# Performance work log

Measured on AMD Instinct MI355X. Metric: run time of the kernel, lower is better.

The kernel has to match this reference:

```python
import jax, jax.numpy as jnp
import numpy as np
from jax import lax

B = 256; C_IN = 12; H = 84; W = 84
HID = 1024; NC = 16; NE = 512; EPC = 64
FLAT = 64 * 7 * 7  # encoder output size for 84x84 input


def setup_inputs() -> dict:
    key = jax.random.key(0)
    ks = jax.random.split(key, 16)
    s = 0.02
    inp = {
        "obs": jax.random.normal(ks[0], (B, C_IN, H, W), dtype=jnp.float32),
        "k1": jax.random.normal(ks[1], (32, C_IN, 8, 8), dtype=jnp.float32) * s,
        "cb1": jnp.zeros((32,), jnp.float32),
        "k2": jax.random.normal(ks[2], (64, 32, 4, 4), dtype=jnp.float32) * s,
        "cb2": jnp.zeros((64,), jnp.float32),
        "k3": jax.random.normal(ks[3], (64, 64, 3, 3), dtype=jnp.float32) * s,
        "cb3": jnp.zeros((64,), jnp.float32),
        "Wproj": jax.random.normal(ks[4], (FLAT, HID), dtype=jnp.float32) * s,
        "bproj": jnp.zeros((HID,), jnp.float32),
        "Wcat": jax.random.normal(ks[5], (HID, NC), dtype=jnp.float32) * s,
        "bcat": jnp.zeros((NC,), jnp.float32),
        "W1": jax.random.normal(ks[6], (NC, HID, HID // 2), dtype=jnp.float32) * s,
        "b1": jnp.zeros((NC, HID // 2), jnp.float32),
        "W2": jax.random.normal(ks[7], (NC, HID // 2, EPC), dtype=jnp.float32) * s,
        "b2": jnp.zeros((NC, EPC), jnp.float32),
        "mapping": jax.random.randint(ks[8], (NC, EPC), 0, NE, dtype=jnp.int64)
        if jax.config.jax_enable_x64 else jax.random.randint(ks[8], (NC, EPC), 0, NE, dtype=jnp.int32),
    }
    return inp


def _conv(x, k, b, stride):
    y = lax.conv_general_dilated(x, k, (stride, stride), "VALID",
                                 dimension_numbers=("NCHW", "OIHW", "NCHW"))
    return y + b[None, :, None, None]


def reference(obs, k1, cb1, k2, cb2, k3, cb3, Wproj, bproj, Wcat, bcat,
              W1, b1, W2, b2, mapping):
    # --- CNN encoder ---
    x = jax.nn.relu(_conv(obs, k1, cb1, 4))   # [B,32,20,20]
    x = jax.nn.relu(_conv(x, k2, cb2, 2))     # [B,64,9,9]
    x = jax.nn.relu(_conv(x, k3, cb3, 1))     # [B,64,7,7]
    feats = x.reshape(x.shape[0], -1)          # [B,3136]

    hidden = jax.nn.relu(feats @ Wproj + bproj)          # [B,HID]
    category_logits = hidden @ Wcat + bcat               # [B,NC]
    category_probs = jax.nn.softmax(category_logits, axis=-1)

    # --- batched per-category expert heads (fused) ---
    h1 = jax.nn.relu(jnp.einsum("bh,chm->bcm", hidden, W1) + b1)   # [B,NC,HID/2]
    local = jax.nn.sigmoid(jnp.einsum("bcm,cme->bce", h1, W2) + b2)  # [B,NC,EPC]
    weighted = category_probs[:, :, None] * local                    # [B,NC,EPC]

    # scatter-add into global expert buffer; mapping [NC,EPC] broadcasts to [B,NC,EPC]
    expert_probs = jnp.zeros((hidden.shape[0], NE), hidden.dtype)
    expert_probs = expert_probs.at[:, mapping].add(weighted)

    return category_logits, expert_probs, hidden
```

## Files before the change

### kernel.cpp

```cpp
#include <hip/hip_runtime.h>
#include <hip/hip_bf16.h>


#define B_    256
#define CIN   12
#define HH    84
#define WW    84
#define HID   1024
#define NC    16
#define NE    512
#define EPC   64
#define FLAT  3136

typedef short short8 __attribute__((ext_vector_type(8)));
typedef short short4_t __attribute__((ext_vector_type(4)));
typedef float f32x4 __attribute__((ext_vector_type(4)));

__device__ __forceinline__ short f2bf(float x) {
    unsigned int u = __float_as_uint(x);
    u = (u + 0x7FFFu + ((u >> 16) & 1u)) >> 16;
    return (short)u;
}

__global__ __launch_bounds__(256) void prep_weights_kernel(
        const float* __restrict__ k1, const float* __restrict__ k2,
        const float* __restrict__ k3, short* __restrict__ k1bf,
        short* __restrict__ k2t, short* __restrict__ k3t) {
    int i = blockIdx.x * 256 + threadIdx.x;
    if (i < 24576) {
        k1bf[i] = f2bf(k1[i]);
    } else if (i < 24576 + 32768) {
        int j = i - 24576;
        int oc = j >> 9, rem = j & 511, tap = rem >> 5, ic = rem & 31;
        k2t[j] = f2bf(k2[oc * 512 + ic * 16 + tap]);
    } else if (i < 24576 + 32768 + 36864) {
        int j = i - 57344;
        int oc = j / 576, rem = j % 576, tap = rem >> 6, ic = rem & 63;
        k3t[j] = f2bf(k3[oc * 576 + ic * 9 + tap]);
    }
}

__global__ __launch_bounds__(256) void transpose_cast_kernel(
        const float* __restrict__ src, short* __restrict__ dst,
        int R, int C, long sbs, long dbs) {
    __shared__ float tile[32][33];
    const int c0 = blockIdx.x * 32, r0 = blockIdx.y * 32, z = blockIdx.z;
    const int tx = threadIdx.x & 31, ty = threadIdx.x >> 5;
    const float* s = src + (size_t)z * sbs;
    short* d = dst + (size_t)z * dbs;
    #pragma unroll
    for (int it = 0; it < 4; ++it)
        tile[ty + it * 8][tx] = s[(size_t)(r0 + ty + it * 8) * C + c0 + tx];
    __syncthreads();
    #pragma unroll
    for (int it = 0; it < 4; ++it) {
        int j = ty + it * 8;
        d[(size_t)(c0 + j) * R + r0 + tx] = f2bf(tile[tx][j]);
    }
}

__global__ __launch_bounds__(448) void conv1_mfma_kernel(
        const float* __restrict__ obs, const short* __restrict__ k1bf,
        const float* __restrict__ cb1, short* __restrict__ x1bf) {
    __shared__ short slab[CIN][24][88];
    const int oyq = blockIdx.x, b = blockIdx.y;
    const int tid = threadIdx.x;

    const float* src = obs + (size_t)b * (CIN * HH * WW) + (20 * oyq) * WW;
    for (int l = tid; l < CIN * 24 * 21; l += 448) {
        int ic = l / 504, rem = l % 504, r = rem / 21, c4 = rem % 21;
        float4 f = *(const float4*)(src + (size_t)ic * (HH * WW) + r * WW + 4 * c4);
        short4_t v;
        v[0] = f2bf(f.x); v[1] = f2bf(f.y); v[2] = f2bf(f.z); v[3] = f2bf(f.w);
        *(short4_t*)&slab[ic][r][4 * c4] = v;
    }
    __syncthreads();

    const int w = tid >> 6, l = tid & 63, lr = l & 15, g = l >> 4;
    const int p = w * 16 + lr;
    const int pw = (p < 100) ? p : 99;
    const int oy_l = pw / 20, ox = pw % 20;
    const short* bb0 = k1bf + lr * 768;
    const short* bb1 = k1bf + (16 + lr) * 768;

    f32x4 acc0 = {0.f, 0.f, 0.f, 0.f}, acc1 = {0.f, 0.f, 0.f, 0.f};
    #pragma unroll 4
    for (int s = 0; s < 24; ++s) {
        const int idx = s * 4 + g;
        const int ic = idx >> 3, ky = idx & 7;
        const short* ap = &slab[ic][4 * oy_l + ky][4 * ox];
        short8 a;
        *(short4_t*)&a       = *(const short4_t*)ap;
        *((short4_t*)&a + 1) = *(const short4_t*)(ap + 4);
        short8 b0 = *(const short8*)(bb0 + s * 32 + g * 8);
        short8 b1 = *(const short8*)(bb1 + s * 32 + g * 8);
        acc0 = __builtin_amdgcn_mfma_f32_16x16x32_bf16(a, b0, acc0, 0, 0, 0);
        acc1 = __builtin_amdgcn_mfma_f32_16x16x32_bf16(a, b1, acc1, 0, 0, 0);
    }
    const float c0v = cb1[lr], c1v = cb1[16 + lr];
    #pragma unroll
    for (int r = 0; r < 4; ++r) {
        const int ro = w * 16 + g * 4 + r;
        if (ro < 100) {
            const int oy_g = 5 * oyq + ro / 20, ox_g = ro % 20;
            short* dst = x1bf + ((size_t)(b * 20 + oy_g) * 20 + ox_g) * 32;
            dst[lr]      = f2bf(fmaxf(acc0[r] + c0v, 0.f));
            dst[16 + lr] = f2bf(fmaxf(acc1[r] + c1v, 0.f));
        }
    }
}

__global__ __launch_bounds__(64) void conv2_mfma_kernel(
        const short* __restrict__ x1bf, const short* __restrict__ k2t,
        const float* __restrict__ cb2, short* __restrict__ x2bf) {
    const int l = threadIdx.x, lr = l & 15, g = l >> 4;
    const int mfb = blockIdx.x * 16;
    const int ro = mfb + lr;
    const int b = ro / 81, pp = ro % 81, oy = pp / 9, ox = pp % 9;
    const short* abase = x1bf + (size_t)b * 12800;

    f32x4 acc[4] = {};
    #pragma unroll 4
    for (int s = 0; s < 16; ++s) {
        const int ky = s >> 2, kx = s & 3;
        short8 a = *(const short8*)(abase +
            ((size_t)((2 * oy + ky) * 20 + 2 * ox + kx)) * 32 + g * 8);
        #pragma unroll
        for (int nf = 0; nf < 4; ++nf) {
            short8 bv = *(const short8*)(k2t + (size_t)(nf * 16 + lr) * 512 + s * 32 + g * 8);
            acc[nf] = __builtin_amdgcn_mfma_f32_16x16x32_bf16(a, bv, acc[nf], 0, 0, 0);
        }
    }
    #pragma unroll
    for (int nf = 0; nf < 4; ++nf) {
        const int col = nf * 16 + lr;
        const float bb = cb2[col];
        #pragma unroll
        for (int r = 0; r < 4; ++r) {
            const int roo = mfb + g * 4 + r;
            x2bf[(size_t)roo * 64 + col] = f2bf(fmaxf(acc[nf][r] + bb, 0.f));
        }
    }
}

__global__ __launch_bounds__(64) void conv3_mfma_kernel(
        const short* __restrict__ x2bf, const short* __restrict__ k3t,
        const float* __restrict__ cb3, short* __restrict__ featsbf) {
    const int l = threadIdx.x, lr = l & 15, g = l >> 4;
    const int mfb = blockIdx.x * 16;
    const int ro = mfb + lr;
    const int b = ro / 49, pp = ro % 49, oy = pp / 7, ox = pp % 7;
    const short* abase = x2bf + (size_t)b * 5184;

    f32x4 acc[4] = {};
    #pragma unroll 4
    for (int s = 0; s < 18; ++s) {
        const int tap = s >> 1, ich = s & 1;
        const int ky = tap / 3, kx = tap % 3;
        short8 a = *(const short8*)(abase +
            ((size_t)((oy + ky) * 9 + ox + kx)) * 64 + ich * 32 + g * 8);
        #pragma unroll
        for (int nf = 0; nf < 4; ++nf) {
            short8 bv = *(const short8*)(k3t + (size_t)(nf * 16 + lr) * 576 + s * 32 + g * 8);
            acc[nf] = __builtin_amdgcn_mfma_f32_16x16x32_bf16(a, bv, acc[nf], 0, 0, 0);
        }
    }
    #pragma unroll
    for (int nf = 0; nf < 4; ++nf) {
        const int col = nf * 16 + lr;
        const float bb = cb3[col];
        #pragma unroll
        for (int r = 0; r < 4; ++r) {
            const int roo = mfb + g * 4 + r;
            const int b_o = roo / 49, p_o = roo % 49;
            featsbf[(size_t)b_o * FLAT + col * 49 + p_o] =
                f2bf(fmaxf(acc[nf][r] + bb, 0.f));
        }
    }
}

__global__ __launch_bounds__(64) void proj_mfma_kernel(
        const short* __restrict__ Abf, const short* __restrict__ Wt,
        const float* __restrict__ bproj, float* __restrict__ hidden,
        short* __restrict__ hbf) {
    const int l = threadIdx.x, lr = l & 15, g = l >> 4;
    const int n0 = blockIdx.x * 16, m0 = blockIdx.y * 32;
    const short* a0 = Abf + (size_t)(m0 + lr) * FLAT;
    const short* a1 = Abf + (size_t)(m0 + 16 + lr) * FLAT;
    const short* br = Wt + (size_t)(n0 + lr) * FLAT;

    f32x4 acc0 = {}, acc1 = {};
    #pragma unroll 4
    for (int s = 0; s < 98; ++s) {
        const int k = s * 32 + g * 8;
        short8 bv = *(const short8*)(br + k);
        short8 av0 = *(const short8*)(a0 + k);
        short8 av1 = *(const short8*)(a1 + k);
        acc0 = __builtin_amdgcn_mfma_f32_16x16x32_bf16(av0, bv, acc0, 0, 0, 0);
        acc1 = __builtin_amdgcn_mfma_f32_16x16x32_bf16(av1, bv, acc1, 0, 0, 0);
    }
    const int col = n0 + lr;
    const float bb = bproj[col];
    #pragma unroll
    for (int r = 0; r < 4; ++r) {
        const int m = m0 + g * 4 + r;
        float v = fmaxf(acc0[r] + bb, 0.f);
        hidden[(size_t)m * HID + col] = v;
        hbf[(size_t)m * HID + col] = f2bf(v);
        const int m2 = m + 16;
        float v2 = fmaxf(acc1[r] + bb, 0.f);
        hidden[(size_t)m2 * HID + col] = v2;
        hbf[(size_t)m2 * HID + col] = f2bf(v2);
    }
}

__global__ __launch_bounds__(256) void cat_softmax_kernel(
        const float* __restrict__ hidden, const float* __restrict__ Wcat,
        const float* __restrict__ bcat, float* __restrict__ logits,
        float* __restrict__ probs) {
    __shared__ float red[256];
    __shared__ float lvals[16];
    const int b = blockIdx.x, tid = threadIdx.x;
    const int cc = tid & 15, kq = tid >> 4;
    const float* hrow = hidden + (size_t)b * HID;
    float p = 0.f;
    for (int t = 0; t < 64; ++t) {
        int k = kq * 64 + t;
        p += hrow[k] * Wcat[k * NC + cc];
    }
    red[tid] = p;
    __syncthreads();
    if (tid < 16) {
        float s = bcat[tid];
        #pragma unroll
        for (int q = 0; q < 16; ++q) s += red[q * 16 + tid];
        logits[b * NC + tid] = s;
        lvals[tid] = s;
    }
    __syncthreads();
    if (tid < 16) {
        float m = lvals[0];
        #pragma unroll
        for (int q = 1; q < 16; ++q) m = fmaxf(m, lvals[q]);
        float sum = 0.f;
        #pragma unroll
        for (int q = 0; q < 16; ++q) sum += expf(lvals[q] - m);
        probs[b * NC + tid] = expf(lvals[tid] - m) / sum;
    }
}

__global__ __launch_bounds__(64) void expert1_mfma_kernel(
        const short* __restrict__ Hbf, const short* __restrict__ W1t,
        const float* __restrict__ b1, short* __restrict__ h1bf) {
    const int l = threadIdx.x, lr = l & 15, g = l >> 4;
    const int n0 = blockIdx.x * 32, m0 = blockIdx.y * 64, c = blockIdx.z;
    const short* ar[4];
    #pragma unroll
    for (int i = 0; i < 4; ++i) ar[i] = Hbf + (size_t)(m0 + i * 16 + lr) * HID;
    const short* br0 = W1t + (size_t)c * (512 * HID) + (size_t)(n0 + lr) * HID;
    const short* br1 = br0 + 16 * HID;

    f32x4 acc[4][2] = {};
    #pragma unroll 2
    for (int s = 0; s < 32; ++s) {
        const int k = s * 32 + g * 8;
        short8 b0 = *(const short8*)(br0 + k);
        short8 b1v = *(const short8*)(br1 + k);
        #pragma unroll
        for (int i = 0; i < 4; ++i) {
            short8 a = *(const short8*)(ar[i] + k);
            acc[i][0] = __builtin_amdgcn_mfma_f32_16x16x32_bf16(a, b0, acc[i][0], 0, 0, 0);
            acc[i][1] = __builtin_amdgcn_mfma_f32_16x16x32_bf16(a, b1v, acc[i][1], 0, 0, 0);
        }
    }
    #pragma unroll
    for (int j = 0; j < 2; ++j) {
        const int col = n0 + j * 16 + lr;
        const float bb = b1[c * 512 + col];
        #pragma unroll
        for (int i = 0; i < 4; ++i)
            #pragma unroll
            for (int r = 0; r < 4; ++r) {
                const int m = m0 + i * 16 + g * 4 + r;
                h1bf[((size_t)c * B_ + m) * 512 + col] =
                    f2bf(fmaxf(acc[i][j][r] + bb, 0.f));
            }
    }
}

__global__ __launch_bounds__(64) void expert2_mfma_kernel(
        const short* __restrict__ h1bf, const short* __restrict__ W2t,
        const float* __restrict__ b2, const float* __restrict__ probs,
        const int* __restrict__ mapping, float* __restrict__ outexp) {
    const int l = threadIdx.x, lr = l & 15, g = l >> 4;
    const int mfb = blockIdx.x * 16, c = blockIdx.y;
    const short* ar = h1bf + ((size_t)c * B_ + mfb + lr) * 512;
    const short* wb = W2t + (size_t)c * (EPC * 512);

    f32x4 acc[4] = {};
    #pragma unroll 4
    for (int s = 0; s < 16; ++s) {
        const int k = s * 32 + g * 8;
        short8 a = *(const short8*)(ar + k);
        #pragma unroll
        for (int nf = 0; nf < 4; ++nf) {
            short8 bv = *(const short8*)(wb + (size_t)(nf * 16 + lr) * 512 + k);
            acc[nf] = __builtin_amdgcn_mfma_f32_16x16x32_bf16(a, bv, acc[nf], 0, 0, 0);
        }
    }
    #pragma unroll
    for (int nf = 0; nf < 4; ++nf) {
        const int e = nf * 16 + lr;
        const float bb = b2[c * EPC + e];
        const int tgt = mapping[c * EPC + e];
        #pragma unroll
        for (int r = 0; r < 4; ++r) {
            const int m = mfb + g * 4 + r;
            const float v = probs[m * NC + c] / (1.f + expf(-(acc[nf][r] + bb)));
            atomicAdd(&outexp[(size_t)m * NE + tgt], v);
        }
    }
}

extern "C" void kernel_launch(void* const* d_in, const int* in_sizes, int n_in,
                              void* d_out, int out_size, void* d_ws, size_t ws_size,
                              hipStream_t stream) {
    const float* obs   = (const float*)d_in[0];
    const float* k1    = (const float*)d_in[1];
    const float* cb1   = (const float*)d_in[2];
    const float* k2    = (const float*)d_in[3];
    const float* cb2   = (const float*)d_in[4];
    const float* k3    = (const float*)d_in[5];
    const float* cb3   = (const float*)d_in[6];
    const float* Wproj = (const float*)d_in[7];
    const float* bproj = (const float*)d_in[8];
    const float* Wcat  = (const float*)d_in[9];
    const float* bcat  = (const float*)d_in[10];
    const float* W1    = (const float*)d_in[11];
    const float* b1    = (const float*)d_in[12];
    const float* W2    = (const float*)d_in[13];
    const float* b2    = (const float*)d_in[14];
    const int*   mapping = (const int*)d_in[15];

    float* out    = (float*)d_out;
    float* logits = out;
    float* outexp = out + B_ * NC;
    float* hidden = out + B_ * NC + B_ * NE;

    char* ws = (char*)d_ws;
    short* x1bf    = (short*)ws;
    short* Wprojt  = (short*)ws;
    short* W1t     = (short*)ws;
    short* W2t     = (short*)ws;
    short* x2bf    = (short*)(ws + 6553600);
    short* featsbf = (short*)(ws + 9207808);
    short* hidbf   = (short*)(ws + 16777216);
    float* probs   = (float*)(ws + 17301504);
    short* k1bf    = (short*)(ws + 17317888);
    short* k2t     = (short*)(ws + 17367040);
    short* k3t     = (short*)(ws + 17432576);
    short* h1bf    = (short*)(ws + 17506304);

    hipMemsetAsync(outexp, 0, (size_t)B_ * NE * sizeof(float), stream);

    prep_weights_kernel<<<dim3(368), 256, 0, stream>>>(k1, k2, k3, k1bf, k2t, k3t);
    conv1_mfma_kernel<<<dim3(4, B_), 448, 0, stream>>>(obs, k1bf, cb1, x1bf);
    conv2_mfma_kernel<<<dim3(1296), 64, 0, stream>>>(x1bf, k2t, cb2, x2bf);
    transpose_cast_kernel<<<dim3(32, 98, 1), 256, 0, stream>>>(
        Wproj, Wprojt, FLAT, HID, 0, 0);
    conv3_mfma_kernel<<<dim3(784), 64, 0, stream>>>(x2bf, k3t, cb3, featsbf);
    proj_mfma_kernel<<<dim3(64, 8), 64, 0, stream>>>(featsbf, Wprojt, bproj, hidden, hidbf);
    cat_softmax_kernel<<<dim3(B_), 256, 0, stream>>>(hidden, Wcat, bcat, logits, probs);
    transpose_cast_kernel<<<dim3(16, 32, 16), 256, 0, stream>>>(
        W1, W1t, HID, 512, (long)HID * 512, (long)HID * 512);
    expert1_mfma_kernel<<<dim3(16, 4, 16), 64, 0, stream>>>(hidbf, W1t, b1, h1bf);
    transpose_cast_kernel<<<dim3(2, 16, 16), 256, 0, stream>>>(
        W2, W2t, 512, EPC, (long)512 * EPC, (long)512 * EPC);
    expert2_mfma_kernel<<<dim3(16, 16), 64, 0, stream>>>(
        h1bf, W2t, b2, probs, mapping, outexp);
}
```

Measured before the change: 373.7 us.

## Split-K the projection GEMM, shrink expert tiles, batch conv1 slab loads

The projection GEMM is split into 8 K-chunks over a 3D grid that atomically accumulate into a zeroed fp32 buffer. A new epilogue kernel then applies bias, ReLU and the bf16 cast. Expert1 and expert2 use smaller per-block tiles so more blocks run in parallel. Conv1's slab load issues seven float4 loads before converting and storing, to raise memory-level parallelism. The cost is an extra memset, an extra kernel launch, atomic traffic, less register reuse per block, and split-K results that are no longer bitwise deterministic.

Result: no change. 375.7 us (+0.5%).

```diff
diff --git a/kernel.cpp b/kernel.cpp
--- a/kernel.cpp
+++ b/kernel.cpp
@@ -67,12 +67,30 @@
     const int tid = threadIdx.x;
 
     const float* src = obs + (size_t)b * (CIN * HH * WW) + (20 * oyq) * WW;
-    for (int l = tid; l < CIN * 24 * 21; l += 448) {
-        int ic = l / 504, rem = l % 504, r = rem / 21, c4 = rem % 21;
-        float4 f = *(const float4*)(src + (size_t)ic * (HH * WW) + r * WW + 4 * c4);
-        short4_t v;
-        v[0] = f2bf(f.x); v[1] = f2bf(f.y); v[2] = f2bf(f.z); v[3] = f2bf(f.w);
-        *(short4_t*)&slab[ic][r][4 * c4] = v;
+    short* sl = &slab[0][0][0];
+    #pragma unroll
+    for (int ph = 0; ph < 2; ++ph) {
+        float4 v[7];
+        int dsti[7];
+        #pragma unroll
+        for (int it = 0; it < 7; ++it) {
+            int l = ph * 3136 + it * 448 + tid;
+            int ok = (l < 6048);
+            int li = ok ? l : 6047;
+            int ic = li / 504, rem = li - ic * 504;
+            int r = rem / 21, c4 = rem - r * 21;
+            v[it] = *(const float4*)(src + (size_t)ic * (HH * WW) + r * WW + 4 * c4);
+            dsti[it] = ok ? (ic * (24 * 88) + r * 88 + 4 * c4) : -1;
+        }
+        #pragma unroll
+        for (int it = 0; it < 7; ++it) {
+            if (dsti[it] >= 0) {
+                short4_t s4v;
+                s4v[0] = f2bf(v[it].x); s4v[1] = f2bf(v[it].y);
+                s4v[2] = f2bf(v[it].z); s4v[3] = f2bf(v[it].w);
+                *(short4_t*)(sl + dsti[it]) = s4v;
+            }
+        }
     }
     __syncthreads();
 
@@ -181,37 +199,45 @@
 
 __global__ __launch_bounds__(64) void proj_mfma_kernel(
         const short* __restrict__ Abf, const short* __restrict__ Wt,
-        const float* __restrict__ bproj, float* __restrict__ hidden,
-        short* __restrict__ hbf) {
+        float* __restrict__ haccum) {
     const int l = threadIdx.x, lr = l & 15, g = l >> 4;
-    const int n0 = blockIdx.x * 16, m0 = blockIdx.y * 32;
-    const short* a0 = Abf + (size_t)(m0 + lr) * FLAT;
-    const short* a1 = Abf + (size_t)(m0 + 16 + lr) * FLAT;
-    const short* br = Wt + (size_t)(n0 + lr) * FLAT;
-
-    f32x4 acc0 = {}, acc1 = {};
-    #pragma unroll 4
-    for (int s = 0; s < 98; ++s) {
+    const int n0 = blockIdx.x * 64, m0 = blockIdx.y * 16;
+    const int kz = blockIdx.z;
+    const int s0 = (kz * 98) >> 3, s1 = ((kz + 1) * 98) >> 3;
+    const short* ar = Abf + (size_t)(m0 + lr) * FLAT;
+    const short* br0 = Wt + (size_t)(n0 + lr) * FLAT;
+
+    f32x4 acc[4] = {};
+    #pragma unroll 2
+    for (int s = s0; s < s1; ++s) {
         const int k = s * 32 + g * 8;
-        short8 bv = *(const short8*)(br + k);
-        short8 av0 = *(const short8*)(a0 + k);
-        short8 av1 = *(const short8*)(a1 + k);
-        acc0 = __builtin_amdgcn_mfma_f32_16x16x32_bf16(av0, bv, acc0, 0, 0, 0);
-        acc1 = __builtin_amdgcn_mfma_f32_16x16x32_bf16(av1, bv, acc1, 0, 0, 0);
-    }
-    const int col = n0 + lr;
-    const float bb = bproj[col];
-    #pragma unroll
-    for (int r = 0; r < 4; ++r) {
-        const int m = m0 + g * 4 + r;
-        float v = fmaxf(acc0[r] + bb, 0.f);
-        hidden[(size_t)m * HID + col] = v;
-        hbf[(size_t)m * HID + col] = f2bf(v);
-        const int m2 = m + 16;
-        float v2 = fmaxf(acc1[r] + bb, 0.f);
-        hidden[(size_t)m2 * HID + col] = v2;
-        hbf[(size_t)m2 * HID + col] = f2bf(v2);
-    }
+        short8 a = *(const short8*)(ar + k);
+        #pragma unroll
+        for (int nf = 0; nf < 4; ++nf) {
+            short8 bv = *(const short8*)(br0 + (size_t)nf * 16 * FLAT + k);
+            acc[nf] = __builtin_amdgcn_mfma_f32_16x16x32_bf16(a, bv, acc[nf], 0, 0, 0);
+        }
+    }
+    #pragma unroll
+    for (int nf = 0; nf < 4; ++nf)
+        #pragma unroll
+        for (int r = 0; r < 4; ++r)
+            atomicAdd(&haccum[(size_t)(m0 + g * 4 + r) * HID + n0 + nf * 16 + lr],
+                      acc[nf][r]);
+}
+
+__global__ __launch_bounds__(256) void proj_epi2_kernel(
+        const float* __restrict__ haccum, const float* __restrict__ bproj,
+        float* __restrict__ hidden, short* __restrict__ hbf) {
+    const int i = blockIdx.x * 256 + threadIdx.x;
+    float4 v = *(const float4*)&haccum[4 * i];
+    float4 bb = *(const float4*)&bproj[(4 * i) & (HID - 1)];
+    float4 r;
+    r.x = fmaxf(v.x + bb.x, 0.f); r.y = fmaxf(v.y + bb.y, 0.f);
+    r.z = fmaxf(v.z + bb.z, 0.f); r.w = fmaxf(v.w + bb.w, 0.f);
+    *(float4*)&hidden[4 * i] = r;
+    short4_t h; h[0] = f2bf(r.x); h[1] = f2bf(r.y); h[2] = f2bf(r.z); h[3] = f2bf(r.w);
+    *(short4_t*)&hbf[4 * i] = h;
 }
 
 __global__ __launch_bounds__(256) void cat_softmax_kernel(
@@ -253,32 +279,31 @@
         const short* __restrict__ Hbf, const short* __restrict__ W1t,
         const float* __restrict__ b1, short* __restrict__ h1bf) {
     const int l = threadIdx.x, lr = l & 15, g = l >> 4;
-    const int n0 = blockIdx.x * 32, m0 = blockIdx.y * 64, c = blockIdx.z;
-    const short* ar[4];
-    #pragma unroll
-    for (int i = 0; i < 4; ++i) ar[i] = Hbf + (size_t)(m0 + i * 16 + lr) * HID;
+    const int n0 = blockIdx.x * 32, m0 = blockIdx.y * 32, c = blockIdx.z;
+    const short* ar0 = Hbf + (size_t)(m0 + lr) * HID;
+    const short* ar1 = ar0 + (size_t)16 * HID;
     const short* br0 = W1t + (size_t)c * (512 * HID) + (size_t)(n0 + lr) * HID;
-    const short* br1 = br0 + 16 * HID;
-
-    f32x4 acc[4][2] = {};
-    #pragma unroll 2
+    const short* br1 = br0 + (size_t)16 * HID;
+
+    f32x4 acc[2][2] = {};
+    #pragma unroll 4
     for (int s = 0; s < 32; ++s) {
         const int k = s * 32 + g * 8;
-        short8 b0 = *(const short8*)(br0 + k);
+        short8 a0 = *(const short8*)(ar0 + k);
+        short8 a1 = *(const short8*)(ar1 + k);
+        short8 b0v = *(const short8*)(br0 + k);
         short8 b1v = *(const short8*)(br1 + k);
-        #pragma unroll
-        for (int i = 0; i < 4; ++i) {
-            short8 a = *(const short8*)(ar[i] + k);
-            acc[i][0] = __builtin_amdgcn_mfma_f32_16x16x32_bf16(a, b0, acc[i][0], 0, 0, 0);
-            acc[i][1] = __builtin_amdgcn_mfma_f32_16x16x32_bf16(a, b1v, acc[i][1], 0, 0, 0);
-        }
+        acc[0][0] = __builtin_amdgcn_mfma_f32_16x16x32_bf16(a0, b0v, acc[0][0], 0, 0, 0);
+        acc[0][1] = __builtin_amdgcn_mfma_f32_16x16x32_bf16(a0, b1v, acc[0][1], 0, 0, 0);
+        acc[1][0] = __builtin_amdgcn_mfma_f32_16x16x32_bf16(a1, b0v, acc[1][0], 0, 0, 0);
+        acc[1][1] = __builtin_amdgcn_mfma_f32_16x16x32_bf16(a1, b1v, acc[1][1], 0, 0, 0);
     }
     #pragma unroll
     for (int j = 0; j < 2; ++j) {
         const int col = n0 + j * 16 + lr;
         const float bb = b1[c * 512 + col];
         #pragma unroll
-        for (int i = 0; i < 4; ++i)
+        for (int i = 0; i < 2; ++i)
             #pragma unroll
             for (int r = 0; r < 4; ++r) {
                 const int m = m0 + i * 16 + g * 4 + r;
@@ -293,32 +318,26 @@
         const float* __restrict__ b2, const float* __restrict__ probs,
         const int* __restrict__ mapping, float* __restrict__ outexp) {
     const int l = threadIdx.x, lr = l & 15, g = l >> 4;
-    const int mfb = blockIdx.x * 16, c = blockIdx.y;
-    const short* ar = h1bf + ((size_t)c * B_ + mfb + lr) * 512;
-    const short* wb = W2t + (size_t)c * (EPC * 512);
-
-    f32x4 acc[4] = {};
+    const int m0 = blockIdx.x * 16, n0 = blockIdx.y * 16, c = blockIdx.z;
+    const short* ar = h1bf + ((size_t)c * B_ + m0 + lr) * 512;
+    const short* br = W2t + (size_t)c * (EPC * 512) + (size_t)(n0 + lr) * 512;
+
+    f32x4 acc = {};
     #pragma unroll 4
     for (int s = 0; s < 16; ++s) {
         const int k = s * 32 + g * 8;
         short8 a = *(const short8*)(ar + k);
-        #pragma unroll
-        for (int nf = 0; nf < 4; ++nf) {
-            short8 bv = *(const short8*)(wb + (size_t)(nf * 16 + lr) * 512 + k);
-            acc[nf] = __builtin_amdgcn_mfma_f32_16x16x32_bf16(a, bv, acc[nf], 0, 0, 0);
-        }
-    }
-    #pragma unroll
-    for (int nf = 0; nf < 4; ++nf) {
-        const int e = nf * 16 + lr;
-        const float bb = b2[c * EPC + e];
-        const int tgt = mapping[c * EPC + e];
-        #pragma unroll
-        for (int r = 0; r < 4; ++r) {
-            const int m = mfb + g * 4 + r;
-            const float v = probs[m * NC + c] / (1.f + expf(-(acc[nf][r] + bb)));
-            atomicAdd(&outexp[(size_t)m * NE + tgt], v);
-        }
+        short8 bv = *(const short8*)(br + k);
+        acc = __builtin_amdgcn_mfma_f32_16x16x32_bf16(a, bv, acc, 0, 0, 0);
+    }
+    const int e = n0 + lr;
+    const float bb = b2[c * EPC + e];
+    const int tgt = mapping[c * EPC + e];
+    #pragma unroll
+    for (int r = 0; r < 4; ++r) {
+        const int m = m0 + g * 4 + r;
+        const float v = probs[m * NC + c] / (1.f + expf(-(acc[r] + bb)));
+        atomicAdd(&outexp[(size_t)m * NE + tgt], v);
     }
 }
 
@@ -353,6 +372,7 @@
     short* W1t     = (short*)ws;
     short* W2t     = (short*)ws;
     short* x2bf    = (short*)(ws + 6553600);
+    float* haccum  = (float*)(ws + 6553600);
     short* featsbf = (short*)(ws + 9207808);
     short* hidbf   = (short*)(ws + 16777216);
     float* probs   = (float*)(ws + 17301504);
@@ -369,13 +389,15 @@
     transpose_cast_kernel<<<dim3(32, 98, 1), 256, 0, stream>>>(
         Wproj, Wprojt, FLAT, HID, 0, 0);
     conv3_mfma_kernel<<<dim3(784), 64, 0, stream>>>(x2bf, k3t, cb3, featsbf);
-    proj_mfma_kernel<<<dim3(64, 8), 64, 0, stream>>>(featsbf, Wprojt, bproj, hidden, hidbf);
+    hipMemsetAsync(haccum, 0, (size_t)B_ * HID * sizeof(float), stream);
+    proj_mfma_kernel<<<dim3(16, 16, 8), 64, 0, stream>>>(featsbf, Wprojt, haccum);
+    proj_epi2_kernel<<<dim3(256), 256, 0, stream>>>(haccum, bproj, hidden, hidbf);
     cat_softmax_kernel<<<dim3(B_), 256, 0, stream>>>(hidden, Wcat, bcat, logits, probs);
     transpose_cast_kernel<<<dim3(16, 32, 16), 256, 0, stream>>>(
         W1, W1t, HID, 512, (long)HID * 512, (long)HID * 512);
-    expert1_mfma_kernel<<<dim3(16, 4, 16), 64, 0, stream>>>(hidbf, W1t, b1, h1bf);
+    expert1_mfma_kernel<<<dim3(16, 8, 16), 64, 0, stream>>>(hidbf, W1t, b1, h1bf);
     transpose_cast_kernel<<<dim3(2, 16, 16), 256, 0, stream>>>(
         W2, W2t, 512, EPC, (long)512 * EPC, (long)512 * EPC);
-    expert2_mfma_kernel<<<dim3(16, 16), 64, 0, stream>>>(
+    expert2_mfma_kernel<<<dim3(16, 4, 16), 64, 0, stream>>>(
         h1bf, W2t, b2, probs, mapping, outexp);
 }
```
